# Performance work log

Hardware: AMD Instinct MI355X
Metric: run time of the kernel (lower is better)

Reference implementation:

```python
import jax, jax.numpy as jnp
import numpy as np

EPS = 1e-5
B, C, N_A, N_B, P, M = 128, 32, 12, 12, 8192, 2


def _bn(x, gamma, beta, mean, var):
    # x: (B, C, P); per-channel inference batch norm
    scale = gamma * jax.lax.rsqrt(var + EPS)
    return x * scale[None, :, None] + (beta - mean * scale)[None, :, None]


def setup_inputs() -> dict:
    key = jax.random.key(0)
    ks = jax.random.split(key, 12)
    return {
        "feat_a": jax.random.normal(ks[0], (B, C, N_A), jnp.float32),
        "feat_b": jax.random.normal(ks[1], (B, C, N_B), jnp.float32),
        "assign_a": jax.random.randint(ks[2], (P, M), 0, N_A, jnp.int32),
        "assign_b": jax.random.randint(ks[3], (P, M), 0, N_B, jnp.int32),
        "bn1_gamma": jax.random.uniform(ks[4], (C,), jnp.float32, 0.5, 1.5),
        "bn1_beta": jax.random.normal(ks[5], (C,), jnp.float32) * 0.1,
        "bn1_mean": jax.random.normal(ks[6], (C,), jnp.float32) * 0.1,
        "bn1_var": jax.random.uniform(ks[7], (C,), jnp.float32, 0.5, 1.5),
        "conv_w": jax.random.normal(ks[8], (C, C), jnp.float32) / np.sqrt(C),
        "bn2_gamma": jax.random.uniform(ks[9], (C,), jnp.float32, 0.5, 1.5),
        "bn2_beta": jax.random.normal(ks[10], (C,), jnp.float32) * 0.1,
        "bn2_mean": jax.random.normal(ks[11], (C,), jnp.float32) * 0.1,
        "bn2_var": jnp.ones((C,), jnp.float32),
    }


def reference(feat_a, feat_b, assign_a, assign_b,
              bn1_gamma, bn1_beta, bn1_mean, bn1_var,
              conv_w, bn2_gamma, bn2_beta, bn2_mean, bn2_var):
    # Gather product features via permutation indices: (B, C, P, M)
    ga = feat_a[:, :, assign_a].max(axis=-1)  # max over constituents -> (B, C, P)
    gb = feat_b[:, :, assign_b].max(axis=-1)
    agg = jnp.maximum(ga, gb)                 # 'max' aggregation across products
    x = _bn(agg, bn1_gamma, bn1_beta, bn1_mean, bn1_var)
    x = jnp.einsum('oc,bcp->bop', conv_w, x)  # 1x1 Conv1d, no bias
    x = _bn(x, bn2_gamma, bn2_beta, bn2_mean, bn2_var)
    return jax.nn.relu(x)
```

## Files before the change

kernel.cpp:

```cpp
#include <hip/hip_runtime.h>


#define EPS 1e-5f
constexpr int B  = 128;
constexpr int C  = 32;
constexpr int NA = 12;
constexpr int PP = 8192;
constexpr int PT = 256;
constexpr int FS = 36;

__global__ __launch_bounds__(256) void fold_kernel(
    const float* __restrict__ conv_w,
    const float* __restrict__ g1, const float* __restrict__ b1,
    const float* __restrict__ m1, const float* __restrict__ v1,
    const float* __restrict__ g2, const float* __restrict__ b2,
    const float* __restrict__ m2, const float* __restrict__ v2,
    float* __restrict__ wpp, float* __restrict__ bpp)
{
    __shared__ float s1[C], t1[C], s2[C], t2[C];
    int tid = threadIdx.x;
    if (tid < C) {
        float s = g1[tid] * rsqrtf(v1[tid] + EPS);
        s1[tid] = s;
        t1[tid] = b1[tid] - m1[tid] * s;
        float ss = g2[tid] * rsqrtf(v2[tid] + EPS);
        s2[tid] = ss;
        t2[tid] = b2[tid] - m2[tid] * ss;
    }
    __syncthreads();
    for (int i = tid; i < C * C; i += 256) {
        int o = i >> 5, c = i & 31;
        wpp[i] = conv_w[i] * s1[c] * s2[o];
    }
    if (tid < C) {
        float acc = 0.f;
        for (int c = 0; c < C; ++c) acc += conv_w[tid * C + c] * t1[c];
        bpp[tid] = acc * s2[tid] + t2[tid];
    }
}

__global__ __launch_bounds__(256) void main_kernel(
    const float* __restrict__ feat_a, const float* __restrict__ feat_b,
    const int*   __restrict__ assign_a, const int* __restrict__ assign_b,
    const float* __restrict__ wpp, const float* __restrict__ bpp,
    float* __restrict__ out)
{
    __shared__ float fa[NA * FS];
    __shared__ float fb[NA * FS];

    const int tid = threadIdx.x;
    const int b  = blockIdx.x >> 5;
    const int p0 = (blockIdx.x & 31) * PT;

    for (int i = tid; i < C * NA; i += 256) {
        int c = i / NA, n = i - c * NA;
        fa[n * FS + c] = feat_a[b * C * NA + i];
        fb[n * FS + c] = feat_b[b * C * NA + i];
    }
    __syncthreads();

    const int p = p0 + tid;
    const int2 ia = ((const int2*)assign_a)[p];
    const int2 ib = ((const int2*)assign_b)[p];

    const float* ra0 = &fa[ia.x * FS];
    const float* ra1 = &fa[ia.y * FS];
    const float* rb0 = &fb[ib.x * FS];
    const float* rb1 = &fb[ib.y * FS];

    float x[C];
#pragma unroll
    for (int cc = 0; cc < C; cc += 4) {
        float4 va0 = *(const float4*)(ra0 + cc);
        float4 va1 = *(const float4*)(ra1 + cc);
        float4 vb0 = *(const float4*)(rb0 + cc);
        float4 vb1 = *(const float4*)(rb1 + cc);
        x[cc + 0] = fmaxf(fmaxf(va0.x, va1.x), fmaxf(vb0.x, vb1.x));
        x[cc + 1] = fmaxf(fmaxf(va0.y, va1.y), fmaxf(vb0.y, vb1.y));
        x[cc + 2] = fmaxf(fmaxf(va0.z, va1.z), fmaxf(vb0.z, vb1.z));
        x[cc + 3] = fmaxf(fmaxf(va0.w, va1.w), fmaxf(vb0.w, vb1.w));
    }

    float* outp = out + b * C * PP + p;
#pragma unroll 4
    for (int o = 0; o < C; ++o) {
        float acc = bpp[o];
#pragma unroll
        for (int c = 0; c < C; ++c)
            acc = fmaf(wpp[o * C + c], x[c], acc);
        outp[o * PP] = fmaxf(acc, 0.f);
    }
}

extern "C" void kernel_launch(void* const* d_in, const int* in_sizes, int n_in,
                              void* d_out, int out_size, void* d_ws, size_t ws_size,
                              hipStream_t stream) {
    const float* feat_a   = (const float*)d_in[0];
    const float* feat_b   = (const float*)d_in[1];
    const int*   assign_a = (const int*)  d_in[2];
    const int*   assign_b = (const int*)  d_in[3];
    const float* g1 = (const float*)d_in[4];
    const float* b1 = (const float*)d_in[5];
    const float* m1 = (const float*)d_in[6];
    const float* v1 = (const float*)d_in[7];
    const float* cw = (const float*)d_in[8];
    const float* g2 = (const float*)d_in[9];
    const float* b2 = (const float*)d_in[10];
    const float* m2 = (const float*)d_in[11];
    const float* v2 = (const float*)d_in[12];

    float* out = (float*)d_out;
    float* wpp = (float*)d_ws;
    float* bpp = wpp + C * C;

    fold_kernel<<<1, 256, 0, stream>>>(cw, g1, b1, m1, v1, g2, b2, m2, v2, wpp, bpp);
    main_kernel<<<B * (PP / PT), 256, 0, stream>>>(feat_a, feat_b, assign_a, assign_b,
                                                   wpp, bpp, out);
}
```

Before: 201.1 us.

## Process two points per thread and stage folded weights in shared memory

Each block now covers 512 points with 256 threads, so every thread computes two output columns and reuses each weight load for both. The folded weights and bias are copied into shared memory and read as float4 instead of coming from global memory inside the FMA loop. Launch bounds now ask for 4 blocks per SM. The two 32-float register arrays raise register pressure, and the grid is half as large.

```diff
diff --git a/kernel.cpp b/kernel.cpp
--- a/kernel.cpp
+++ b/kernel.cpp
@@ -6,7 +6,7 @@
 constexpr int C  = 32;
 constexpr int NA = 12;
 constexpr int PP = 8192;
-constexpr int PT = 256;
+constexpr int PT = 512;
 constexpr int FS = 36;
 
 __global__ __launch_bounds__(256) void fold_kernel(
@@ -39,7 +39,7 @@
     }
 }
 
-__global__ __launch_bounds__(256) void main_kernel(
+__global__ __launch_bounds__(256, 4) void main_kernel(
     const float* __restrict__ feat_a, const float* __restrict__ feat_b,
     const int*   __restrict__ assign_a, const int* __restrict__ assign_b,
     const float* __restrict__ wpp, const float* __restrict__ bpp,
@@ -47,10 +47,15 @@
 {
     __shared__ float fa[NA * FS];
     __shared__ float fb[NA * FS];
+    __shared__ float wsh[C * C];
+    __shared__ float bsh[C];
 
     const int tid = threadIdx.x;
-    const int b  = blockIdx.x >> 5;
-    const int p0 = (blockIdx.x & 31) * PT;
+    const int b  = blockIdx.x >> 4;
+    const int p0 = (blockIdx.x & 15) * PT;
+
+    for (int i = tid; i < C * C; i += 256) wsh[i] = wpp[i];
+    if (tid < C) bsh[tid] = bpp[tid];
 
     for (int i = tid; i < C * NA; i += 256) {
         int c = i / NA, n = i - c * NA;
@@ -59,36 +64,65 @@
     }
     __syncthreads();
 
-    const int p = p0 + tid;
-    const int2 ia = ((const int2*)assign_a)[p];
-    const int2 ib = ((const int2*)assign_b)[p];
+    const int pA = p0 + tid;
+    const int pB = pA + 256;
+    const int2 ia0 = ((const int2*)assign_a)[pA];
+    const int2 ib0 = ((const int2*)assign_b)[pA];
+    const int2 ia1 = ((const int2*)assign_a)[pB];
+    const int2 ib1 = ((const int2*)assign_b)[pB];
 
-    const float* ra0 = &fa[ia.x * FS];
-    const float* ra1 = &fa[ia.y * FS];
-    const float* rb0 = &fb[ib.x * FS];
-    const float* rb1 = &fb[ib.y * FS];
-
-    float x[C];
+    float x0[C], x1[C];
+    {
+        const float* a0 = &fa[ia0.x * FS];
+        const float* a1 = &fa[ia0.y * FS];
+        const float* b0 = &fb[ib0.x * FS];
+        const float* b1 = &fb[ib0.y * FS];
+        const float* a2 = &fa[ia1.x * FS];
+        const float* a3 = &fa[ia1.y * FS];
+        const float* b2 = &fb[ib1.x * FS];
+        const float* b3 = &fb[ib1.y * FS];
 #pragma unroll
-    for (int cc = 0; cc < C; cc += 4) {
-        float4 va0 = *(const float4*)(ra0 + cc);
-        float4 va1 = *(const float4*)(ra1 + cc);
-        float4 vb0 = *(const float4*)(rb0 + cc);
-        float4 vb1 = *(const float4*)(rb1 + cc);
-        x[cc + 0] = fmaxf(fmaxf(va0.x, va1.x), fmaxf(vb0.x, vb1.x));
-        x[cc + 1] = fmaxf(fmaxf(va0.y, va1.y), fmaxf(vb0.y, vb1.y));
-        x[cc + 2] = fmaxf(fmaxf(va0.z, va1.z), fmaxf(vb0.z, vb1.z));
-        x[cc + 3] = fmaxf(fmaxf(va0.w, va1.w), fmaxf(vb0.w, vb1.w));
+        for (int cc = 0; cc < C; cc += 4) {
+            float4 va0 = *(const float4*)(a0 + cc);
+            float4 va1 = *(const float4*)(a1 + cc);
+            float4 vb0 = *(const float4*)(b0 + cc);
+            float4 vb1 = *(const float4*)(b1 + cc);
+            x0[cc + 0] = fmaxf(fmaxf(va0.x, va1.x), fmaxf(vb0.x, vb1.x));
+            x0[cc + 1] = fmaxf(fmaxf(va0.y, va1.y), fmaxf(vb0.y, vb1.y));
+            x0[cc + 2] = fmaxf(fmaxf(va0.z, va1.z), fmaxf(vb0.z, vb1.z));
+            x0[cc + 3] = fmaxf(fmaxf(va0.w, va1.w), fmaxf(vb0.w, vb1.w));
+            float4 wa0 = *(const float4*)(a2 + cc);
+            float4 wa1 = *(const float4*)(a3 + cc);
+            float4 wb0 = *(const float4*)(b2 + cc);
+            float4 wb1 = *(const float4*)(b3 + cc);
+            x1[cc + 0] = fmaxf(fmaxf(wa0.x, wa1.x), fmaxf(wb0.x, wb1.x));
+            x1[cc + 1] = fmaxf(fmaxf(wa0.y, wa1.y), fmaxf(wb0.y, wb1.y));
+            x1[cc + 2] = fmaxf(fmaxf(wa0.z, wa1.z), fmaxf(wb0.z, wb1.z));
+            x1[cc + 3] = fmaxf(fmaxf(wa0.w, wa1.w), fmaxf(wb0.w, wb1.w));
+        }
     }
 
-    float* outp = out + b * C * PP + p;
-#pragma unroll 4
+    float* out0 = out + b * C * PP + pA;
+    float* out1 = out + b * C * PP + pB;
+#pragma unroll 2
     for (int o = 0; o < C; ++o) {
-        float acc = bpp[o];
+        const float* wr = &wsh[o * C];
+        float acc0 = bsh[o];
+        float acc1 = acc0;
 #pragma unroll
-        for (int c = 0; c < C; ++c)
-            acc = fmaf(wpp[o * C + c], x[c], acc);
-        outp[o * PP] = fmaxf(acc, 0.f);
+        for (int c = 0; c < C; c += 4) {
+            float4 w = *(const float4*)(wr + c);
+            acc0 = fmaf(w.x, x0[c + 0], acc0);
+            acc1 = fmaf(w.x, x1[c + 0], acc1);
+            acc0 = fmaf(w.y, x0[c + 1], acc0);
+            acc1 = fmaf(w.y, x1[c + 1], acc1);
+            acc0 = fmaf(w.z, x0[c + 2], acc0);
+            acc1 = fmaf(w.z, x1[c + 2], acc1);
+            acc0 = fmaf(w.w, x0[c + 3], acc0);
+            acc1 = fmaf(w.w, x1[c + 3], acc1);
+        }
+        out0[o * PP] = fmaxf(acc0, 0.f);
+        out1[o * PP] = fmaxf(acc1, 0.f);
     }
 }
 
```

Measured after the change: 175.8 us. -12.6%, faster.

## Compute 1x1 conv with split-bf16 MFMA instead of scalar FP32 FMAs

Applied to the files above, without the earlier changes.

Replaces the per-thread 32x32 scalar FMA loop with bf16 MFMA 16x16x32 instructions. To keep near-FP32 accuracy it uses three products per tile: hi*hi, hi*lo and lo*hi. The fold kernel pre-splits the folded weights into hi/lo bf16 fragments laid out for MFMA. The main kernel stages the gathered features as hi/lo bf16 rows in shared memory before the matrix multiply. This adds an extra barrier and more LDS traffic, and the output is still written as FP32, so a memory-bound kernel may see little benefit.

```diff
diff --git a/kernel.cpp b/kernel.cpp
--- a/kernel.cpp
+++ b/kernel.cpp
@@ -8,6 +8,22 @@
 constexpr int PP = 8192;
 constexpr int PT = 256;
 constexpr int FS = 36;
+constexpr int XS = 40;
+
+typedef short bfv8  __attribute__((ext_vector_type(8)));
+typedef float f32x4 __attribute__((ext_vector_type(4)));
+
+__device__ __forceinline__ ushort f2bf(float f) {
+    uint u = __float_as_uint(f);
+    u += 0x7fffu + ((u >> 16) & 1u);
+    return (ushort)(u >> 16);
+}
+__device__ __forceinline__ float bf2f(ushort h) {
+    return __uint_as_float(((uint)h) << 16);
+}
+__device__ __forceinline__ uint pk(ushort lo, ushort hi) {
+    return (uint)lo | ((uint)hi << 16);
+}
 
 __global__ __launch_bounds__(256) void fold_kernel(
     const float* __restrict__ conv_w,
@@ -15,9 +31,10 @@
     const float* __restrict__ m1, const float* __restrict__ v1,
     const float* __restrict__ g2, const float* __restrict__ b2,
     const float* __restrict__ m2, const float* __restrict__ v2,
-    float* __restrict__ wpp, float* __restrict__ bpp)
+    ushort* __restrict__ afh, ushort* __restrict__ afl,
+    float* __restrict__ bpp)
 {
-    __shared__ float s1[C], t1[C], s2[C], t2[C];
+    __shared__ float s1[C], t1[C], s2[C], t2[C], w2[C * C];
     int tid = threadIdx.x;
     if (tid < C) {
         float s = g1[tid] * rsqrtf(v1[tid] + EPS);
@@ -30,65 +47,128 @@
     __syncthreads();
     for (int i = tid; i < C * C; i += 256) {
         int o = i >> 5, c = i & 31;
-        wpp[i] = conv_w[i] * s1[c] * s2[o];
+        w2[i] = conv_w[i] * s1[c] * s2[o];
     }
     if (tid < C) {
         float acc = 0.f;
         for (int c = 0; c < C; ++c) acc += conv_w[tid * C + c] * t1[c];
         bpp[tid] = acc * s2[tid] + t2[tid];
     }
+    __syncthreads();
+#pragma unroll
+    for (int e = tid * 4; e < tid * 4 + 4; ++e) {
+        int t = e >> 9, l = (e >> 3) & 63, j = e & 7;
+        int m = (l & 15) + 16 * t;
+        int k = (l >> 4) * 8 + j;
+        float w = w2[m * C + k];
+        ushort h = f2bf(w);
+        afh[e] = h;
+        afl[e] = f2bf(w - bf2f(h));
+    }
 }
 
 __global__ __launch_bounds__(256) void main_kernel(
     const float* __restrict__ feat_a, const float* __restrict__ feat_b,
     const int*   __restrict__ assign_a, const int* __restrict__ assign_b,
-    const float* __restrict__ wpp, const float* __restrict__ bpp,
+    const ushort* __restrict__ afh, const ushort* __restrict__ afl,
+    const float* __restrict__ bpp,
     float* __restrict__ out)
 {
-    __shared__ float fa[NA * FS];
-    __shared__ float fb[NA * FS];
-
-    const int tid = threadIdx.x;
-    const int b  = blockIdx.x >> 5;
-    const int p0 = (blockIdx.x & 31) * PT;
+    __shared__ __align__(16) float  fa[NA * FS];
+    __shared__ __align__(16) float  fb[NA * FS];
+    __shared__ __align__(16) ushort xh[PT * XS];
+    __shared__ __align__(16) ushort xl[PT * XS];
+
+    const int tid  = threadIdx.x;
+    const int lane = tid & 63;
+    const int b    = blockIdx.x >> 5;
+    const int p0   = (blockIdx.x & 31) * PT;
+    const int q    = lane >> 4;
+    const int n    = lane & 15;
+
+    bfv8 ah0 = *(const bfv8*)(afh + lane * 8);
+    bfv8 ah1 = *(const bfv8*)(afh + 512 + lane * 8);
+    bfv8 al0 = *(const bfv8*)(afl + lane * 8);
+    bfv8 al1 = *(const bfv8*)(afl + 512 + lane * 8);
+    float bias0[4], bias1[4];
+#pragma unroll
+    for (int r = 0; r < 4; ++r) {
+        bias0[r] = bpp[q * 4 + r];
+        bias1[r] = bpp[16 + q * 4 + r];
+    }
 
     for (int i = tid; i < C * NA; i += 256) {
-        int c = i / NA, n = i - c * NA;
-        fa[n * FS + c] = feat_a[b * C * NA + i];
-        fb[n * FS + c] = feat_b[b * C * NA + i];
-    }
-    __syncthreads();
-
-    const int p = p0 + tid;
-    const int2 ia = ((const int2*)assign_a)[p];
-    const int2 ib = ((const int2*)assign_b)[p];
-
-    const float* ra0 = &fa[ia.x * FS];
-    const float* ra1 = &fa[ia.y * FS];
-    const float* rb0 = &fb[ib.x * FS];
-    const float* rb1 = &fb[ib.y * FS];
-
-    float x[C];
-#pragma unroll
-    for (int cc = 0; cc < C; cc += 4) {
-        float4 va0 = *(const float4*)(ra0 + cc);
-        float4 va1 = *(const float4*)(ra1 + cc);
-        float4 vb0 = *(const float4*)(rb0 + cc);
-        float4 vb1 = *(const float4*)(rb1 + cc);
-        x[cc + 0] = fmaxf(fmaxf(va0.x, va1.x), fmaxf(vb0.x, vb1.x));
-        x[cc + 1] = fmaxf(fmaxf(va0.y, va1.y), fmaxf(vb0.y, vb1.y));
-        x[cc + 2] = fmaxf(fmaxf(va0.z, va1.z), fmaxf(vb0.z, vb1.z));
-        x[cc + 3] = fmaxf(fmaxf(va0.w, va1.w), fmaxf(vb0.w, vb1.w));
-    }
-
-    float* outp = out + b * C * PP + p;
-#pragma unroll 4
-    for (int o = 0; o < C; ++o) {
-        float acc = bpp[o];
-#pragma unroll
-        for (int c = 0; c < C; ++c)
-            acc = fmaf(wpp[o * C + c], x[c], acc);
-        outp[o * PP] = fmaxf(acc, 0.f);
+        int c = i / NA, nn = i - c * NA;
+        fa[nn * FS + c] = feat_a[b * C * NA + i];
+        fb[nn * FS + c] = feat_b[b * C * NA + i];
+    }
+    __syncthreads();
+
+    {
+        const int p = p0 + tid;
+        const int2 ia = ((const int2*)assign_a)[p];
+        const int2 ib = ((const int2*)assign_b)[p];
+        const float* a0 = &fa[ia.x * FS];
+        const float* a1 = &fa[ia.y * FS];
+        const float* c0 = &fb[ib.x * FS];
+        const float* c1 = &fb[ib.y * FS];
+
+        float x[C];
+#pragma unroll
+        for (int cc = 0; cc < C; cc += 4) {
+            float4 va0 = *(const float4*)(a0 + cc);
+            float4 va1 = *(const float4*)(a1 + cc);
+            float4 vb0 = *(const float4*)(c0 + cc);
+            float4 vb1 = *(const float4*)(c1 + cc);
+            x[cc + 0] = fmaxf(fmaxf(va0.x, va1.x), fmaxf(vb0.x, vb1.x));
+            x[cc + 1] = fmaxf(fmaxf(va0.y, va1.y), fmaxf(vb0.y, vb1.y));
+            x[cc + 2] = fmaxf(fmaxf(va0.z, va1.z), fmaxf(vb0.z, vb1.z));
+            x[cc + 3] = fmaxf(fmaxf(va0.w, va1.w), fmaxf(vb0.w, vb1.w));
+        }
+
+        ushort* rowh = &xh[tid * XS];
+        ushort* rowl = &xl[tid * XS];
+#pragma unroll
+        for (int c = 0; c < C; c += 8) {
+            ushort h[8], l[8];
+#pragma unroll
+            for (int j = 0; j < 8; ++j) {
+                float v = x[c + j];
+                h[j] = f2bf(v);
+                l[j] = f2bf(v - bf2f(h[j]));
+            }
+            uint4 vh = make_uint4(pk(h[0], h[1]), pk(h[2], h[3]),
+                                  pk(h[4], h[5]), pk(h[6], h[7]));
+            uint4 vl = make_uint4(pk(l[0], l[1]), pk(l[2], l[3]),
+                                  pk(l[4], l[5]), pk(l[6], l[7]));
+            *(uint4*)(rowh + c) = vh;
+            *(uint4*)(rowl + c) = vl;
+        }
+    }
+    __syncthreads();
+
+    const int wave = tid >> 6;
+    const f32x4 zero = {0.f, 0.f, 0.f, 0.f};
+    float* outb = out + b * C * PP + p0;
+#pragma unroll
+    for (int ch = 0; ch < 4; ++ch) {
+        const int base = (wave * 4 + ch) * 16;
+        const bfv8 bh = *(const bfv8*)&xh[(base + n) * XS + q * 8];
+        const bfv8 bl = *(const bfv8*)&xl[(base + n) * XS + q * 8];
+
+        f32x4 d0 = __builtin_amdgcn_mfma_f32_16x16x32_bf16(ah0, bh, zero, 0, 0, 0);
+        d0       = __builtin_amdgcn_mfma_f32_16x16x32_bf16(ah0, bl, d0,   0, 0, 0);
+        d0       = __builtin_amdgcn_mfma_f32_16x16x32_bf16(al0, bh, d0,   0, 0, 0);
+        f32x4 d1 = __builtin_amdgcn_mfma_f32_16x16x32_bf16(ah1, bh, zero, 0, 0, 0);
+        d1       = __builtin_amdgcn_mfma_f32_16x16x32_bf16(ah1, bl, d1,   0, 0, 0);
+        d1       = __builtin_amdgcn_mfma_f32_16x16x32_bf16(al1, bh, d1,   0, 0, 0);
+
+        float* op = outb + base + n;
+#pragma unroll
+        for (int r = 0; r < 4; ++r) {
+            op[(q * 4 + r) * PP]      = fmaxf(d0[r] + bias0[r], 0.f);
+            op[(16 + q * 4 + r) * PP] = fmaxf(d1[r] + bias1[r], 0.f);
+        }
     }
 }
 
@@ -110,10 +190,13 @@
     const float* v2 = (const float*)d_in[12];
 
     float* out = (float*)d_out;
-    float* wpp = (float*)d_ws;
-    float* bpp = wpp + C * C;
-
-    fold_kernel<<<1, 256, 0, stream>>>(cw, g1, b1, m1, v1, g2, b2, m2, v2, wpp, bpp);
-    main_kernel<<<B * (PP / PT), 256, 0, stream>>>(feat_a, feat_b, assign_a, assign_b,
-                                                   wpp, bpp, out);
-}
+    ushort* afh = (ushort*)d_ws;
+    ushort* afl = (ushort*)((char*)d_ws + 2048);
+    float*  bpp = (float*)((char*)d_ws + 4096);
+
+    fold_kernel<<<1, 256, 0, stream>>>(cw, g1, b1, m1, v1, g2, b2, m2, v2,
+                                       afh, afl, bpp);
+    main_kernel<<<B * (PP / PT), 256, 0, stream>>>(feat_a, feat_b,
+                                                   assign_a, assign_b,
+                                                   afh, afl, bpp, out);
+}
```

After: 174.5 us. 1.15x faster.
